# Optimization experiments

Measured on AMD Instinct MI355X. Metric: run time of the kernel, lower is better.

## Reference

```python
import jax, jax.numpy as jnp
import numpy as np

B, H_TRAJ, S = 8, 16, 64
DIM, C = 128, 2000
D = 2 * DIM            # transformer d_model
NUM_HEADS, WINDOW, L = 4, 4, 2
D_FF = 4 * D


def setup_inputs() -> dict:
    key = jax.random.key(0)
    ks = jax.random.split(key, 12)
    w = lambda k, shape, s: jax.random.normal(k, shape, jnp.float32) * s
    return {
        "history": jax.random.randint(ks[0], (B, H_TRAJ, S), 0, C + 1),
        "current_trajectory": jax.random.randint(ks[1], (B, S), 0, C + 1),
        "embedding": w(ks[2], (1, C, DIM), 1.0),
        "null_embedding": jax.random.uniform(ks[3], (D,), jnp.float32),
        "gcn_w": w(ks[4], (DIM, DIM), 0.05),
        "gcn_b": jnp.zeros((DIM,), jnp.float32),
        "enc_attn_w": w(ks[5], (L, 4, D, D), 0.05),
        "enc_attn_b": jnp.zeros((L, 4, D), jnp.float32),
        "enc_ffn_w1": w(ks[6], (L, D, D_FF), 0.05),
        "enc_ffn_b1": jnp.zeros((L, D_FF), jnp.float32),
        "enc_ffn_w2": w(ks[7], (L, D_FF, D), 0.05),
        "enc_ffn_b2": jnp.zeros((L, D), jnp.float32),
        "enc_ln_s": jnp.ones((L, 2, D), jnp.float32),
        "enc_ln_b": jnp.zeros((L, 2, D), jnp.float32),
        "wca_w": w(ks[8], (4, D, D), 0.05),
        "wca_b": jnp.zeros((4, D), jnp.float32),
        "ial_w": w(ks[9], (D, DIM), 0.05),
        "ial_b": jnp.zeros((DIM,), jnp.float32),
    }


def _layer_norm(x, s, b, eps=1e-5):
    m = x.mean(-1, keepdims=True)
    v = ((x - m) ** 2).mean(-1, keepdims=True)
    return (x - m) * jax.lax.rsqrt(v + eps) * s + b


def _mha(xq, xkv, w, b, mask):
    # w: (4,d,d) q/k/v/out, b: (4,d); mask additive, broadcast over heads
    d = xq.shape[-1]
    hd = d // NUM_HEADS
    proj = lambda x, i: (x @ w[i] + b[i]).reshape(x.shape[:-1] + (NUM_HEADS, hd))
    q, k, v = proj(xq, 0), proj(xkv, 1), proj(xkv, 2)
    s = jnp.einsum('bqhd,bkhd->bhqk', q, k) / float(np.sqrt(hd))
    s = s + mask[:, None, :, :]
    a = jax.nn.softmax(s, axis=-1)
    o = jnp.einsum('bhqk,bkhd->bqhd', a, v).reshape(xq.shape)
    return o @ w[3] + b[3]


def _get_graph(history):
    # vectorized scatter-add replacement of the python triple loop
    src, dst = history[:, :, :-1], history[:, :, 1:]
    h_idx = jnp.arange(H_TRAJ, dtype=jnp.float32)
    wts = 1.0 + jnp.exp(-0.01 * (H_TRAJ - 1 - h_idx))          # per-trajectory weight
    valid = (src != C) & (dst != C) & (src != dst)
    wv = jnp.where(valid, wts[None, :, None], 0.0)
    sc, dc = jnp.clip(src, 0, C - 1), jnp.clip(dst, 0, C - 1)
    flat = (jnp.arange(B)[:, None, None] * C * C + sc * C + dc).ravel()
    A = jnp.zeros((B * C * C,), jnp.float32).at[flat].add(wv.ravel())
    return A.reshape(B, C, C)


def _mytransform(A):
    A = A + jnp.eye(C, dtype=A.dtype)
    d = jnp.sqrt(A.sum(axis=1))          # torch code: sqrt of dim-1 sums (no inverse)
    return d[:, :, None] * A * d[:, None, :]   # D @ A @ D


def _temporal(seq_len, d):
    t = jnp.arange(seq_len, dtype=jnp.float32)[:, None]
    den = 10000.0 ** (jnp.arange(0, d, 2, dtype=jnp.float32) / d)
    arg = t / den[None, :]
    return jnp.stack([jnp.sin(arg), jnp.cos(arg)], axis=-1).reshape(seq_len, d)


def _fuse(pos, hist, temp, null_emb):
    # pos: (B,C,D); hist: (B,...,S); gather + where fusion
    g = jax.vmap(lambda p, h: p[h])(pos, jnp.clip(hist, 0, C - 1))
    return jnp.where((hist == C)[..., None], null_emb + temp, g + temp)


def _encoder(x, mask, aw, ab, fw1, fb1, fw2, fb2, lns, lnb):
    for l in range(L):
        a = _mha(x, x, aw[l], ab[l], mask)
        x = _layer_norm(x + a, lns[l, 0], lnb[l, 0])
        f = jax.nn.relu(x @ fw1[l] + fb1[l]) @ fw2[l] + fb2[l]
        x = _layer_norm(x + f, lns[l, 1], lnb[l, 1])
    return x


def reference(history, current_trajectory, embedding, null_embedding, gcn_w, gcn_b,
              enc_attn_w, enc_attn_b, enc_ffn_w1, enc_ffn_b1, enc_ffn_w2, enc_ffn_b2,
              enc_ln_s, enc_ln_b, wca_w, wca_b, ial_w, ial_b):
    E = jnp.broadcast_to(embedding, (B, C, DIM))
    A = _mytransform(_get_graph(history))                      # (B,C,C)
    Eg = jax.nn.relu(A @ E @ gcn_w + gcn_b)                    # GCN layer
    pos = jnp.concatenate([E, Eg], axis=-1)                    # (B,C,2*dim)
    temp = _temporal(S, D)
    fh = _fuse(pos, history, temp, null_embedding).reshape(B * H_TRAJ, S, D)
    fc = _fuse(pos, current_trajectory, temp, null_embedding)  # (B,S,D)
    hmask = jnp.broadcast_to(
        jnp.where((history == C)[:, :, None, :], -jnp.inf, 0.0),
        (B, H_TRAJ, S, S)).reshape(B * H_TRAJ, S, S)
    cmask = jnp.broadcast_to(
        jnp.where((current_trajectory == C)[:, None, :], -jnp.inf, 0.0), (B, S, S))
    mh = _encoder(fh, hmask, enc_attn_w, enc_attn_b, enc_ffn_w1, enc_ffn_b1,
                  enc_ffn_w2, enc_ffn_b2, enc_ln_s, enc_ln_b)
    mc = _encoder(fc, cmask, enc_attn_w, enc_attn_b, enc_ffn_w1, enc_ffn_b1,
                  enc_ffn_w2, enc_ffn_b2, enc_ln_s, enc_ln_b)
    cur_rep = jnp.broadcast_to(mc[:, None], (B, H_TRAJ, S, D)).reshape(B * H_TRAJ, S, D)
    i = jnp.arange(S)
    wmask = jnp.where(jnp.abs(i[:, None] - i[None, :]) <= WINDOW, 0.0, -jnp.inf)[None]
    wca = mh + _mha(mh, cur_rep, wca_w, wca_b, wmask)          # window-based cross attn
    wca = wca.reshape(B, H_TRAJ, S, D)
    # information aggregation over the trajectory axis
    scores = jnp.einsum('bhsd,bsd->bhs', wca, mc) / float(np.sqrt(D))
    aw = jax.nn.softmax(scores, axis=1)
    agg = jnp.einsum('bhs,bhsd->bsd', aw, wca)
    final = jax.nn.relu((agg + mc) @ ial_w + ial_b)            # (B,S,dim)
    return final @ embedding[0].T                              # (B,S,C)
```

## Files before the change

### kernel.cpp

```cpp
#include <hip/hip_runtime.h>
#include <hip/hip_bf16.h>
#include <math.h>

#define C_N   2000
#define DIMN  128
#define DM    256
#define B_N   8
#define HT    16
#define S_N   64
#define NSEQ  136
#define DFF   1024
#define NEDGE (B_N*HT*(S_N-1))

typedef __hip_bfloat16 bf16;
typedef short bf16x8 __attribute__((ext_vector_type(8)));
typedef float f32x4  __attribute__((ext_vector_type(4)));

#define GLOAD_LDS16(gp, lp) \
    __builtin_amdgcn_global_load_lds((const __attribute__((address_space(1))) void*)(gp), \
                                     (__attribute__((address_space(3))) void*)(lp), 16, 0, 0)

__device__ __forceinline__ short f2bf(float v) {
    bf16 t = (bf16)v;
    return *reinterpret_cast<short*>(&t);
}


__global__ void k_colsum(const int* __restrict__ hist, float* __restrict__ colsum) {
    int e = blockIdx.x * blockDim.x + threadIdx.x;
    if (e >= NEDGE) return;
    int s = e % (S_N-1); int bh = e / (S_N-1); int h = bh % HT; int b = bh / HT;
    const int* row = hist + (size_t)bh * S_N;
    int src = row[s], dst = row[s+1];
    if (src != C_N && dst != C_N && src != dst) {
        float w = 1.f + expf(-0.01f * (float)(HT - 1 - h));
        atomicAdd(&colsum[b * C_N + dst], w);
    }
}

__global__ void k_dsqrt(float* __restrict__ dv) {
    int i = blockIdx.x * blockDim.x + threadIdx.x;
    if (i < B_N * C_N) dv[i] = sqrtf(1.f + dv[i]);
}

__global__ void k_initX(const float* __restrict__ dv, const float* __restrict__ E,
                        float* __restrict__ X) {
    size_t i = (size_t)blockIdx.x * 256 + threadIdx.x;
    int k = (int)(i % DIMN); size_t bc = i / DIMN;
    int c = (int)(bc % C_N); int b = (int)(bc / C_N);
    float dd = dv[b * C_N + c];
    X[i] = dd * dd * E[(size_t)c * DIMN + k];
}

__global__ void k_edgeX(const int* __restrict__ hist, const float* __restrict__ dv,
                        const float* __restrict__ E, float* __restrict__ X) {
    int e = blockIdx.x;
    int s = e % (S_N-1); int bh = e / (S_N-1); int h = bh % HT; int b = bh / HT;
    const int* row = hist + (size_t)bh * S_N;
    int src = row[s], dst = row[s+1];
    if (src == C_N || dst == C_N || src == dst) return;
    float w = (1.f + expf(-0.01f * (float)(HT - 1 - h))) * dv[b*C_N+src] * dv[b*C_N+dst];
    int k = threadIdx.x;
    atomicAdd(&X[((size_t)b * C_N + src) * DIMN + k], w * E[(size_t)dst * DIMN + k]);
}


__global__ void k_tobf(const float* __restrict__ s, bf16* __restrict__ d, int n) {
    int i = (blockIdx.x * 256 + threadIdx.x) * 4;
    if (i >= n) return;
    float4 v = *(const float4*)(s + i);
    d[i]   = (bf16)v.x; d[i+1] = (bf16)v.y; d[i+2] = (bf16)v.z; d[i+3] = (bf16)v.w;
}

__global__ void k_transp(const float* __restrict__ src, bf16* __restrict__ dst, int K, int N) {
    __shared__ float t[32][33];
    int mat = blockIdx.z;
    const float* s = src + (size_t)mat * K * N;
    bf16* d = dst + (size_t)mat * N * K;
    int k0 = blockIdx.y * 32, n0 = blockIdx.x * 32;
    #pragma unroll
    for (int j = 0; j < 32; j += 8)
        t[threadIdx.y + j][threadIdx.x] = s[(size_t)(k0 + threadIdx.y + j) * N + n0 + threadIdx.x];
    __syncthreads();
    #pragma unroll
    for (int j = 0; j < 32; j += 8)
        d[(size_t)(n0 + threadIdx.y + j) * K + k0 + threadIdx.x] = (bf16)t[threadIdx.x][threadIdx.y + j];
}

template<int EPI>
__global__ __launch_bounds__(256) void k_bgemm(
        const bf16* __restrict__ A, const bf16* __restrict__ Bt,
        const float* __restrict__ bias, const float* __restrict__ resid,
        void* __restrict__ Cout, int M, int N, int K)
{
    __shared__ bf16 As[128 * 64];
    __shared__ bf16 Bs[64 * 64];
    int tid = threadIdx.x;
    int wid = tid >> 6, lane = tid & 63;
    int m0 = blockIdx.y * 128, n0 = blockIdx.x * 64;
    int wr = wid >> 1, wc = wid & 1;
    int lr = lane >> 3, lc = lane & 7;
    int gc = lc ^ lr;
    f32x4 acc[4][2] = {};

    int nkt = K >> 6;
    for (int kt = 0; kt < nkt; ++kt) {
        int kb = kt << 6;
        #pragma unroll
        for (int s = 0; s < 4; ++s) {
            int seg = wid * 4 + s;
            int row = seg * 8 + lr;
            GLOAD_LDS16(A + (size_t)(m0 + row) * K + kb + gc * 8, As + seg * 512);
        }
        #pragma unroll
        for (int s = 0; s < 2; ++s) {
            int seg = wid * 2 + s;
            int row = seg * 8 + lr;
            GLOAD_LDS16(Bt + (size_t)(n0 + row) * K + kb + gc * 8, Bs + seg * 512);
        }
        __syncthreads();
        #pragma unroll
        for (int kk = 0; kk < 2; ++kk) {
            bf16x8 af[4], bfr[2];
            int c = kk * 4 + (lane >> 4);
            #pragma unroll
            for (int m = 0; m < 4; ++m) {
                int row = wr * 64 + m * 16 + (lane & 15);
                af[m] = *(const bf16x8*)(As + row * 64 + (c ^ (row & 7)) * 8);
            }
            #pragma unroll
            for (int n = 0; n < 2; ++n) {
                int row = wc * 32 + n * 16 + (lane & 15);
                bfr[n] = *(const bf16x8*)(Bs + row * 64 + (c ^ (row & 7)) * 8);
            }
            #pragma unroll
            for (int m = 0; m < 4; ++m)
                #pragma unroll
                for (int n = 0; n < 2; ++n)
                    acc[m][n] = __builtin_amdgcn_mfma_f32_16x16x32_bf16(af[m], bfr[n], acc[m][n], 0, 0, 0);
        }
        __syncthreads();
    }
    int cl = lane & 15, ch = lane >> 4;
    #pragma unroll
    for (int n = 0; n < 2; ++n) {
        int col = n0 + wc * 32 + n * 16 + cl;
        float bv = bias[col];
        #pragma unroll
        for (int m = 0; m < 4; ++m) {
            #pragma unroll
            for (int j = 0; j < 4; ++j) {
                int row = m0 + wr * 64 + m * 16 + ch * 4 + j;
                float v = acc[m][n][j] + bv;
                if (EPI & 4) v += resid[(size_t)row * N + col];
                if (EPI & 2) v = fmaxf(v, 0.f);
                if (EPI & 8) ((bf16*)Cout)[(size_t)row * N + col] = (bf16)v;
                else         ((float*)Cout)[(size_t)row * N + col] = v;
            }
        }
    }
}

template<int EPI, bool BTRANS>
__global__ __launch_bounds__(256) void k_gemm(
        const float* __restrict__ A, const float* __restrict__ Bm,
        const float* __restrict__ bias, const float* __restrict__ resid,
        float* __restrict__ Cm, int M, int N, int K)
{
    __shared__ float As[16][65];
    __shared__ float Bs[16][65];
    int tid = threadIdx.x;
    int tx = tid & 15, ty = tid >> 4;
    int m0 = blockIdx.y * 64, n0 = blockIdx.x * 64;
    float acc[4][4] = {};
    for (int k0 = 0; k0 < K; k0 += 16) {
        {
            int mm = tid >> 2;
            int kk = (tid & 3) << 2;
            int m = m0 + mm;
            float4 v = {0,0,0,0};
            if (m < M) v = *(const float4*)(A + (size_t)m * K + k0 + kk);
            As[kk+0][mm] = v.x; As[kk+1][mm] = v.y; As[kk+2][mm] = v.z; As[kk+3][mm] = v.w;
        }
        if (!BTRANS) {
            int kk = tid >> 4;
            int nn = (tid & 15) << 2;
            int n = n0 + nn;
            const float* src = Bm + (size_t)(k0+kk) * N + n;
            float4 v = {0,0,0,0};
            if (n + 3 < N) v = *(const float4*)src;
            else {
                if (n   < N) v.x = src[0];
                if (n+1 < N) v.y = src[1];
                if (n+2 < N) v.z = src[2];
                if (n+3 < N) v.w = src[3];
            }
            Bs[kk][nn] = v.x; Bs[kk][nn+1] = v.y; Bs[kk][nn+2] = v.z; Bs[kk][nn+3] = v.w;
        } else {
            int nn = tid >> 2;
            int kk = (tid & 3) << 2;
            int n = n0 + nn;
            float4 v = {0,0,0,0};
            if (n < N) v = *(const float4*)(Bm + (size_t)n * K + k0 + kk);
            Bs[kk+0][nn] = v.x; Bs[kk+1][nn] = v.y; Bs[kk+2][nn] = v.z; Bs[kk+3][nn] = v.w;
        }
        __syncthreads();
        #pragma unroll
        for (int kk = 0; kk < 16; ++kk) {
            float a[4], b[4];
            #pragma unroll
            for (int i = 0; i < 4; ++i) a[i] = As[kk][ty*4+i];
            #pragma unroll
            for (int j = 0; j < 4; ++j) b[j] = Bs[kk][tx*4+j];
            #pragma unroll
            for (int i = 0; i < 4; ++i)
                #pragma unroll
                for (int j = 0; j < 4; ++j)
                    acc[i][j] = fmaf(a[i], b[j], acc[i][j]);
        }
        __syncthreads();
    }
    #pragma unroll
    for (int i = 0; i < 4; ++i) {
        int m = m0 + ty*4 + i;
        if (m >= M) continue;
        #pragma unroll
        for (int j = 0; j < 4; ++j) {
            int n = n0 + tx*4 + j;
            if (n >= N) continue;
            float v = acc[i][j];
            if (EPI & 1) v += bias[n];
            if (EPI & 4) v += resid[(size_t)m * N + n];
            if (EPI & 2) v = fmaxf(v, 0.f);
            Cm[(size_t)m * N + n] = v;
        }
    }
}


__global__ void k_temp(float* __restrict__ temp) {
    int s = blockIdx.x; int d = threadIdx.x;
    int k = d >> 1;
    float den = powf(10000.f, (2.f * (float)k) / 256.f);
    float arg = (float)s / den;
    temp[s * DM + d] = (d & 1) ? cosf(arg) : sinf(arg);
}

__global__ void k_fuse(const int* __restrict__ hist, const int* __restrict__ cur,
                       const float* __restrict__ E, const float* __restrict__ Eg,
                       const float* __restrict__ nullE, const float* __restrict__ temp,
                       float* __restrict__ Xenc, bf16* __restrict__ Xbf,
                       float* __restrict__ maskb) {
    int blk = blockIdx.x;
    int seq = blk >> 6, s = blk & 63;
    int d = threadIdx.x;
    int idx, b;
    if (seq < 128) { b = seq >> 4; idx = hist[(size_t)seq * S_N + s]; }
    else           { b = seq - 128; idx = cur[b * S_N + s]; }
    float t = temp[s * DM + d];
    float v;
    if (idx == C_N) v = nullE[d] + t;
    else {
        v = ((d < DIMN) ? E[(size_t)idx * DIMN + d]
                        : Eg[((size_t)b * C_N + idx) * DIMN + (d - DIMN)]) + t;
    }
    size_t o = ((size_t)seq * S_N + s) * DM + d;
    Xenc[o] = v;
    Xbf[o]  = (bf16)v;
    if (d == 0) maskb[seq * S_N + s] = (idx == C_N) ? -INFINITY : 0.f;
}

template<bool WCA>
__global__ __launch_bounds__(64) void k_mattn(
        const bf16* __restrict__ Qb, const bf16* __restrict__ Kb,
        const bf16* __restrict__ Vb, const float* __restrict__ maskb,
        bf16* __restrict__ O, int qstr, int kstr)
{
    int seq = blockIdx.x >> 2, head = blockIdx.x & 3;
    int lane = threadIdx.x;
    int cl = lane & 15, ch = lane >> 4;
    __shared__ __align__(16) short VT[64 * 72];
    __shared__ __align__(16) short PT[64 * 72];

    const bf16* Qp = Qb + (size_t)seq * 64 * qstr + head * 64;
    int kvseq = WCA ? (seq >> 4) : seq;
    const bf16* Kp = Kb + (size_t)kvseq * 64 * kstr + head * 64;
    const bf16* Vp = Vb + (size_t)kvseq * 64 * kstr + head * 64;

    bf16x8 aq[4][2], bk[4][2], vr[4][2];
    #pragma unroll
    for (int t = 0; t < 4; ++t)
        #pragma unroll
        for (int kk = 0; kk < 2; ++kk) {
            int row = t * 16 + cl, d0 = kk * 32 + ch * 8;
            aq[t][kk] = *(const bf16x8*)(Qp + (size_t)row * qstr + d0);
            bk[t][kk] = *(const bf16x8*)(Kp + (size_t)row * kstr + d0);
            vr[t][kk] = *(const bf16x8*)(Vp + (size_t)row * kstr + d0);
        }

    f32x4 sa[4][4] = {};
    #pragma unroll
    for (int kk = 0; kk < 2; ++kk)
        #pragma unroll
        for (int m = 0; m < 4; ++m)
            #pragma unroll
            for (int n = 0; n < 4; ++n)
                sa[m][n] = __builtin_amdgcn_mfma_f32_16x16x32_bf16(aq[m][kk], bk[n][kk], sa[m][n], 0, 0, 0);

    #pragma unroll
    for (int t = 0; t < 4; ++t)
        #pragma unroll
        for (int kk = 0; kk < 2; ++kk) {
            int k = t * 16 + cl, d0 = kk * 32 + ch * 8;
            #pragma unroll
            for (int e = 0; e < 8; ++e)
                VT[(d0 + e) * 72 + k] = vr[t][kk][e];
        }

    float mk4[4];
    if (!WCA) {
        #pragma unroll
        for (int n = 0; n < 4; ++n) mk4[n] = maskb[seq * 64 + n * 16 + cl];
    }

    #pragma unroll
    for (int m = 0; m < 4; ++m) {
        #pragma unroll
        for (int j = 0; j < 4; ++j) {
            int q = m * 16 + ch * 4 + j;
            float rm = -INFINITY;
            #pragma unroll
            for (int n = 0; n < 4; ++n) {
                int k = n * 16 + cl;
                float msk = WCA ? ((abs(q - k) <= 4) ? 0.f : -INFINITY) : mk4[n];
                float v = sa[m][n][j] * 0.125f + msk;
                sa[m][n][j] = v;
                rm = fmaxf(rm, v);
            }
            rm = fmaxf(rm, __shfl_xor(rm, 1));
            rm = fmaxf(rm, __shfl_xor(rm, 2));
            rm = fmaxf(rm, __shfl_xor(rm, 4));
            rm = fmaxf(rm, __shfl_xor(rm, 8));
            float rs = 0.f;
            #pragma unroll
            for (int n = 0; n < 4; ++n) {
                float e = expf(sa[m][n][j] - rm);
                sa[m][n][j] = e;
                rs += e;
            }
            rs += __shfl_xor(rs, 1);
            rs += __shfl_xor(rs, 2);
            rs += __shfl_xor(rs, 4);
            rs += __shfl_xor(rs, 8);
            float inv = 1.f / rs;
            #pragma unroll
            for (int n = 0; n < 4; ++n)
                PT[q * 72 + n * 16 + cl] = f2bf(sa[m][n][j] * inv);
        }
    }
    __syncthreads();

    f32x4 oa[4][4] = {};
    #pragma unroll
    for (int kk = 0; kk < 2; ++kk) {
        bf16x8 av[4], bp[4];
        #pragma unroll
        for (int dm = 0; dm < 4; ++dm)
            av[dm] = *(const bf16x8*)(VT + (dm * 16 + cl) * 72 + kk * 32 + ch * 8);
        #pragma unroll
        for (int qn = 0; qn < 4; ++qn)
            bp[qn] = *(const bf16x8*)(PT + (qn * 16 + cl) * 72 + kk * 32 + ch * 8);
        #pragma unroll
        for (int dm = 0; dm < 4; ++dm)
            #pragma unroll
            for (int qn = 0; qn < 4; ++qn)
                oa[dm][qn] = __builtin_amdgcn_mfma_f32_16x16x32_bf16(av[dm], bp[qn], oa[dm][qn], 0, 0, 0);
    }
    __syncthreads();

    #pragma unroll
    for (int dm = 0; dm < 4; ++dm)
        #pragma unroll
        for (int qn = 0; qn < 4; ++qn)
            #pragma unroll
            for (int j = 0; j < 4; ++j)
                PT[(qn * 16 + cl) * 72 + dm * 16 + ch * 4 + j] = f2bf(oa[dm][qn][j]);
    __syncthreads();
    #pragma unroll
    for (int it = 0; it < 8; ++it) {
        int chunk = it * 64 + lane;
        int tok = chunk >> 3, d0 = (chunk & 7) * 8;
        bf16x8 v = *(const bf16x8*)(PT + tok * 72 + d0);
        *(bf16x8*)(O + ((size_t)seq * 64 + tok) * 256 + head * 64 + d0) = v;
    }
}


__global__ __launch_bounds__(256) void k_ln(float* __restrict__ x, const float* __restrict__ a,
                                            const float* __restrict__ s, const float* __restrict__ b,
                                            bf16* __restrict__ xbf) {
    int row = blockIdx.x;
    int d = threadIdx.x;
    size_t idx = (size_t)row * DM + d;
    float v = x[idx] + a[idx];
    __shared__ float red[8];
    float t = v;
    #pragma unroll
    for (int o = 1; o < 64; o <<= 1) t += __shfl_xor(t, o);
    if ((d & 63) == 0) red[d >> 6] = t;
    __syncthreads();
    float mean = (red[0] + red[1] + red[2] + red[3]) * (1.f / 256.f);
    float c = v - mean;
    float t2 = c * c;
    #pragma unroll
    for (int o = 1; o < 64; o <<= 1) t2 += __shfl_xor(t2, o);
    if ((d & 63) == 0) red[4 + (d >> 6)] = t2;
    __syncthreads();
    float var = (red[4] + red[5] + red[6] + red[7]) * (1.f / 256.f);
    float r = c * rsqrtf(var + 1e-5f) * s[d] + b[d];
    x[idx] = r;
    xbf[idx] = (bf16)r;
}


__global__ __launch_bounds__(256) void k_agg(const float* __restrict__ wca,
                                             const float* __restrict__ mc,
                                             float* __restrict__ aggmc) {
    int bs = blockIdx.x; int b = bs >> 6, s = bs & 63;
    int d = threadIdx.x;
    __shared__ float sc[16];
    __shared__ float red[4];
    float mcv = mc[((size_t)b * S_N + s) * DM + d];
    float wv[16];
    #pragma unroll
    for (int h = 0; h < 16; ++h) {
        float w = wca[(((size_t)(b * HT + h)) * S_N + s) * DM + d];
        wv[h] = w;
        float t = w * mcv;
        #pragma unroll
        for (int o = 1; o < 64; o <<= 1) t += __shfl_xor(t, o);
        if ((d & 63) == 0) red[d >> 6] = t;
        __syncthreads();
        if (d == 0) sc[h] = (red[0] + red[1] + red[2] + red[3]) * (1.f / 16.f);
        __syncthreads();
    }
    float mx = -INFINITY;
    #pragma unroll
    for (int h = 0; h < 16; ++h) mx = fmaxf(mx, sc[h]);
    float e[16]; float sum = 0.f;
    #pragma unroll
    for (int h = 0; h < 16; ++h) { e[h] = expf(sc[h] - mx); sum += e[h]; }
    float inv = 1.f / sum;
    float acc = 0.f;
    #pragma unroll
    for (int h = 0; h < 16; ++h) acc += e[h] * inv * wv[h];
    aggmc[((size_t)b * S_N + s) * DM + d] = acc + mcv;
}


extern "C" void kernel_launch(void* const* d_in, const int* in_sizes, int n_in,
                              void* d_out, int out_size, void* d_ws, size_t ws_size,
                              hipStream_t stream) {
    const int*   history = (const int*)d_in[0];
    const int*   cur     = (const int*)d_in[1];
    const float* emb     = (const float*)d_in[2];
    const float* nullE   = (const float*)d_in[3];
    const float* gcn_w   = (const float*)d_in[4];
    const float* gcn_b   = (const float*)d_in[5];
    const float* aw      = (const float*)d_in[6];
    const float* ab      = (const float*)d_in[7];
    const float* fw1     = (const float*)d_in[8];
    const float* fb1     = (const float*)d_in[9];
    const float* fw2     = (const float*)d_in[10];
    const float* fb2     = (const float*)d_in[11];
    const float* lns     = (const float*)d_in[12];
    const float* lnb     = (const float*)d_in[13];
    const float* wca_w   = (const float*)d_in[14];
    const float* wca_b   = (const float*)d_in[15];
    const float* ial_w   = (const float*)d_in[16];
    const float* ial_b   = (const float*)d_in[17];
    float* out = (float*)d_out;
    float* ws  = (float*)d_ws;

    float* dvec   = ws + 0;
    float* maskb  = ws + 16000;
    float* temp   = ws + 24704;
    float* aggmc  = ws + 41088;
    float* finalb = ws + 172160;
    bf16*  wbf    = (bf16*)(ws + 237696);
    float* Xenc   = ws + 1163392;
    bf16*  Xbf    = (bf16*)(ws + 3391616);
    bf16*  Abf    = (bf16*)(ws + 4505728);
    bf16*  Hbf    = (bf16*)(ws + 5619840);
    bf16*  QKVbf  = (bf16*)(ws + 10076288);
    float* O2     = ws + 13418624;
    float* SE     = ws + 15646848;

    bf16* wbf_aw  = wbf;
    bf16* wbf_fw1 = wbf + 524288;
    bf16* wbf_fw2 = wbf + 1048576;
    bf16* wbf_wca = wbf + 1572864;
    bf16* wbf_gcn = wbf + 1835008;

    float* Xg   = O2;
    bf16*  Xgbf = Hbf;
    float* Eg   = SE;
    bf16*  Qwbf = QKVbf;
    bf16*  KVbf = QKVbf + 4194304;

    k_transp<<<dim3(8, 8, 8),  dim3(32, 8), 0, stream>>>(aw,    wbf_aw, 256, 256);
    k_transp<<<dim3(32, 8, 2), dim3(32, 8), 0, stream>>>(fw1,   wbf_fw1, 256, 1024);
    k_transp<<<dim3(8, 32, 2), dim3(32, 8), 0, stream>>>(fw2,   wbf_fw2, 1024, 256);
    k_transp<<<dim3(8, 8, 4),  dim3(32, 8), 0, stream>>>(wca_w, wbf_wca, 256, 256);
    k_transp<<<dim3(4, 4, 1),  dim3(32, 8), 0, stream>>>(gcn_w, wbf_gcn, 128, 128);

    hipMemsetAsync(dvec, 0, 16000 * sizeof(float), stream);
    k_colsum<<<(NEDGE + 255) / 256, 256, 0, stream>>>(history, dvec);
    k_dsqrt<<<(B_N * C_N + 255) / 256, 256, 0, stream>>>(dvec);
    k_initX<<<B_N * C_N * DIMN / 256, 256, 0, stream>>>(dvec, emb, Xg);
    k_edgeX<<<NEDGE, 128, 0, stream>>>(history, dvec, emb, Xg);
    k_tobf<<<2000, 256, 0, stream>>>(Xg, Xgbf, B_N * C_N * DIMN);
    k_bgemm<2><<<dim3(2, 125), 256, 0, stream>>>(Xgbf, wbf_gcn, gcn_b, nullptr, Eg,
                                                 B_N * C_N, DIMN, DIMN);

    k_temp<<<S_N, DM, 0, stream>>>(temp);
    k_fuse<<<NSEQ * S_N, DM, 0, stream>>>(history, cur, emb, Eg, nullE, temp, Xenc, Xbf, maskb);

    for (int l = 0; l < 2; ++l) {
        k_bgemm<9><<<dim3(12, 68), 256, 0, stream>>>(Xbf, wbf_aw + l * 262144,
                ab + l * 1024, nullptr, QKVbf, NSEQ * S_N, 768, 256);
        k_mattn<false><<<NSEQ * 4, 64, 0, stream>>>(QKVbf, QKVbf + 256, QKVbf + 512,
                maskb, Abf, 768, 768);
        k_bgemm<0><<<dim3(4, 68), 256, 0, stream>>>(Abf, wbf_aw + l * 262144 + 196608,
                ab + l * 1024 + 768, nullptr, O2, NSEQ * S_N, 256, 256);
        k_ln<<<NSEQ * S_N, DM, 0, stream>>>(Xenc, O2, lns + (l * 2 + 0) * DM, lnb + (l * 2 + 0) * DM, Xbf);
        k_bgemm<10><<<dim3(16, 68), 256, 0, stream>>>(Xbf, wbf_fw1 + l * 262144,
                fb1 + l * DFF, nullptr, Hbf, NSEQ * S_N, DFF, 256);
        k_bgemm<0><<<dim3(4, 68), 256, 0, stream>>>(Hbf, wbf_fw2 + l * 262144,
                fb2 + l * DM, nullptr, O2, NSEQ * S_N, 256, 1024);
        k_ln<<<NSEQ * S_N, DM, 0, stream>>>(Xenc, O2, lns + (l * 2 + 1) * DM, lnb + (l * 2 + 1) * DM, Xbf);
    }

    float* mh = Xenc;
    bf16*  mc_bf = Xbf + (size_t)128 * S_N * DM;

    k_bgemm<9><<<dim3(4, 64), 256, 0, stream>>>(Xbf, wbf_wca, wca_b, nullptr, Qwbf,
                                                128 * S_N, 256, 256);
    k_bgemm<9><<<dim3(8, 4), 256, 0, stream>>>(mc_bf, wbf_wca + 65536, wca_b + 256, nullptr, KVbf,
                                               B_N * S_N, 512, 256);
    k_mattn<true><<<128 * 4, 64, 0, stream>>>(Qwbf, KVbf, KVbf + 256, nullptr, Abf, 256, 512);
    k_bgemm<4><<<dim3(4, 64), 256, 0, stream>>>(Abf, wbf_wca + 196608, wca_b + 768, mh, SE,
                                                128 * S_N, 256, 256);

    k_agg<<<B_N * S_N, DM, 0, stream>>>(SE, Xenc + (size_t)128 * S_N * DM, aggmc);
    k_gemm<3, false><<<dim3(2, 8), 256, 0, stream>>>(aggmc, ial_w, ial_b, nullptr, finalb,
                                                     B_N * S_N, DIMN, DM);
    k_gemm<0, true><<<dim3(32, 8), 256, 0, stream>>>(finalb, emb, nullptr, nullptr, out,
                                                     B_N * S_N, C_N, DIMN);
}
```

Measured before the change: 380.6 us.

## Reassociate GCN, fuse GEMM with LayerNorm, move tail GEMMs to MFMA

The GCN is reassociated so the embedding is multiplied by the GCN weight once (2000 rows instead of 16000), and the degree scaling and edge scatter are applied to that product, with bias added and ReLU deferred to the fuse kernel. Output-projection and FFN2 GEMMs are fused with the residual add and LayerNorm in a new full-row kernel, which removes the separate LN passes and the O2 round trip. Weight transposes are packed into one launch, the aggregation kernel reduces all 16 scores in one pass instead of syncing per trajectory, and the final two fp32 SIMT GEMMs become bf16 MFMA GEMMs with a padded embedding. The fused LN uses a single-pass variance, and the extra bf16 rounding in the tail may change numerics slightly.

```diff
diff --git a/kernel.cpp b/kernel.cpp
--- a/kernel.cpp
+++ b/kernel.cpp
@@ -38,30 +38,26 @@
     }
 }
 
-__global__ void k_dsqrt(float* __restrict__ dv) {
-    int i = blockIdx.x * blockDim.x + threadIdx.x;
-    if (i < B_N * C_N) dv[i] = sqrtf(1.f + dv[i]);
-}
-
-__global__ void k_initX(const float* __restrict__ dv, const float* __restrict__ E,
-                        float* __restrict__ X) {
+__global__ void k_initX(const float* __restrict__ cs, const float* __restrict__ Y,
+                        const float* __restrict__ gb, float* __restrict__ Eg) {
     size_t i = (size_t)blockIdx.x * 256 + threadIdx.x;
     int k = (int)(i % DIMN); size_t bc = i / DIMN;
     int c = (int)(bc % C_N); int b = (int)(bc / C_N);
-    float dd = dv[b * C_N + c];
-    X[i] = dd * dd * E[(size_t)c * DIMN + k];
-}
-
-__global__ void k_edgeX(const int* __restrict__ hist, const float* __restrict__ dv,
-                        const float* __restrict__ E, float* __restrict__ X) {
+    float dd2 = 1.f + cs[b * C_N + c];
+    Eg[i] = dd2 * Y[(size_t)c * DIMN + k] + gb[k];
+}
+
+__global__ void k_edgeX(const int* __restrict__ hist, const float* __restrict__ cs,
+                        const float* __restrict__ Y, float* __restrict__ Eg) {
     int e = blockIdx.x;
     int s = e % (S_N-1); int bh = e / (S_N-1); int h = bh % HT; int b = bh / HT;
     const int* row = hist + (size_t)bh * S_N;
     int src = row[s], dst = row[s+1];
     if (src == C_N || dst == C_N || src == dst) return;
-    float w = (1.f + expf(-0.01f * (float)(HT - 1 - h))) * dv[b*C_N+src] * dv[b*C_N+dst];
+    float w = (1.f + expf(-0.01f * (float)(HT - 1 - h)))
+            * sqrtf(1.f + cs[b*C_N+src]) * sqrtf(1.f + cs[b*C_N+dst]);
     int k = threadIdx.x;
-    atomicAdd(&X[((size_t)b * C_N + src) * DIMN + k], w * E[(size_t)dst * DIMN + k]);
+    atomicAdd(&Eg[((size_t)b * C_N + src) * DIMN + k], w * Y[(size_t)dst * DIMN + k]);
 }
 
 
@@ -72,26 +68,39 @@
     d[i]   = (bf16)v.x; d[i+1] = (bf16)v.y; d[i+2] = (bf16)v.z; d[i+3] = (bf16)v.w;
 }
 
-__global__ void k_transp(const float* __restrict__ src, bf16* __restrict__ dst, int K, int N) {
+struct TEnt { const float* s; bf16* d; int K; int N; int nm; int tiles; };
+struct TPack { TEnt e[6]; };
+
+__global__ void k_wtpack(TPack p) {
     __shared__ float t[32][33];
-    int mat = blockIdx.z;
-    const float* s = src + (size_t)mat * K * N;
-    bf16* d = dst + (size_t)mat * N * K;
-    int k0 = blockIdx.y * 32, n0 = blockIdx.x * 32;
+    int id = blockIdx.x;
+    TEnt en = p.e[0];
+    #pragma unroll
+    for (int k = 0; k < 6; ++k) {
+        if (id < p.e[k].tiles) { en = p.e[k]; break; }
+        id -= p.e[k].tiles;
+    }
+    int tn = en.N >> 5;
+    int per = (en.K >> 5) * tn;
+    int mat = id / per, t2 = id % per;
+    int ty = t2 / tn, tx = t2 % tn;
+    const float* s = en.s + (size_t)mat * en.K * en.N;
+    bf16* d = en.d + (size_t)mat * en.N * en.K;
+    int k0 = ty * 32, n0 = tx * 32;
     #pragma unroll
     for (int j = 0; j < 32; j += 8)
-        t[threadIdx.y + j][threadIdx.x] = s[(size_t)(k0 + threadIdx.y + j) * N + n0 + threadIdx.x];
+        t[threadIdx.y + j][threadIdx.x] = s[(size_t)(k0 + threadIdx.y + j) * en.N + n0 + threadIdx.x];
     __syncthreads();
     #pragma unroll
     for (int j = 0; j < 32; j += 8)
-        d[(size_t)(n0 + threadIdx.y + j) * K + k0 + threadIdx.x] = (bf16)t[threadIdx.x][threadIdx.y + j];
+        d[(size_t)(n0 + threadIdx.y + j) * en.K + k0 + threadIdx.x] = (bf16)t[threadIdx.x][threadIdx.y + j];
 }
 
 template<int EPI>
 __global__ __launch_bounds__(256) void k_bgemm(
         const bf16* __restrict__ A, const bf16* __restrict__ Bt,
         const float* __restrict__ bias, const float* __restrict__ resid,
-        void* __restrict__ Cout, int M, int N, int K)
+        void* __restrict__ Cout, int M, int N, int K, int ldc, int nreal)
 {
     __shared__ bf16 As[128 * 64];
     __shared__ bf16 Bs[64 * 64];
@@ -145,94 +154,113 @@
     #pragma unroll
     for (int n = 0; n < 2; ++n) {
         int col = n0 + wc * 32 + n * 16 + cl;
-        float bv = bias[col];
+        if ((EPI & 16) && col >= nreal) continue;
+        float bv = (EPI & 1) ? bias[col] : 0.f;
         #pragma unroll
         for (int m = 0; m < 4; ++m) {
             #pragma unroll
             for (int j = 0; j < 4; ++j) {
                 int row = m0 + wr * 64 + m * 16 + ch * 4 + j;
                 float v = acc[m][n][j] + bv;
-                if (EPI & 4) v += resid[(size_t)row * N + col];
+                if (EPI & 4) v += resid[(size_t)row * ldc + col];
                 if (EPI & 2) v = fmaxf(v, 0.f);
-                if (EPI & 8) ((bf16*)Cout)[(size_t)row * N + col] = (bf16)v;
-                else         ((float*)Cout)[(size_t)row * N + col] = v;
-            }
-        }
-    }
-}
-
-template<int EPI, bool BTRANS>
-__global__ __launch_bounds__(256) void k_gemm(
-        const float* __restrict__ A, const float* __restrict__ Bm,
-        const float* __restrict__ bias, const float* __restrict__ resid,
-        float* __restrict__ Cm, int M, int N, int K)
+                if (EPI & 8) ((bf16*)Cout)[(size_t)row * ldc + col] = (bf16)v;
+                else         ((float*)Cout)[(size_t)row * ldc + col] = v;
+            }
+        }
+    }
+}
+
+__global__ __launch_bounds__(256) void k_bgemm_ln(
+        const bf16* __restrict__ A, const bf16* __restrict__ Bt,
+        const float* __restrict__ bias, float* __restrict__ Xf,
+        const float* __restrict__ lns_, const float* __restrict__ lnb_,
+        bf16* __restrict__ Xb, int M, int K)
 {
-    __shared__ float As[16][65];
-    __shared__ float Bs[16][65];
-    int tid = threadIdx.x;
-    int tx = tid & 15, ty = tid >> 4;
-    int m0 = blockIdx.y * 64, n0 = blockIdx.x * 64;
-    float acc[4][4] = {};
-    for (int k0 = 0; k0 < K; k0 += 16) {
-        {
-            int mm = tid >> 2;
-            int kk = (tid & 3) << 2;
-            int m = m0 + mm;
-            float4 v = {0,0,0,0};
-            if (m < M) v = *(const float4*)(A + (size_t)m * K + k0 + kk);
-            As[kk+0][mm] = v.x; As[kk+1][mm] = v.y; As[kk+2][mm] = v.z; As[kk+3][mm] = v.w;
-        }
-        if (!BTRANS) {
-            int kk = tid >> 4;
-            int nn = (tid & 15) << 2;
-            int n = n0 + nn;
-            const float* src = Bm + (size_t)(k0+kk) * N + n;
-            float4 v = {0,0,0,0};
-            if (n + 3 < N) v = *(const float4*)src;
-            else {
-                if (n   < N) v.x = src[0];
-                if (n+1 < N) v.y = src[1];
-                if (n+2 < N) v.z = src[2];
-                if (n+3 < N) v.w = src[3];
-            }
-            Bs[kk][nn] = v.x; Bs[kk][nn+1] = v.y; Bs[kk][nn+2] = v.z; Bs[kk][nn+3] = v.w;
-        } else {
-            int nn = tid >> 2;
-            int kk = (tid & 3) << 2;
-            int n = n0 + nn;
-            float4 v = {0,0,0,0};
-            if (n < N) v = *(const float4*)(Bm + (size_t)n * K + k0 + kk);
-            Bs[kk+0][nn] = v.x; Bs[kk+1][nn] = v.y; Bs[kk+2][nn] = v.z; Bs[kk+3][nn] = v.w;
+    __shared__ bf16 As[64 * 64];
+    __shared__ bf16 Bs[256 * 64];
+    __shared__ float ls1[64][4], ls2[64][4];
+    int tid = threadIdx.x, wid = tid >> 6, lane = tid & 63;
+    int lr = lane >> 3, lc = lane & 7, gc = lc ^ lr;
+    int cl = lane & 15, ch = lane >> 4;
+    int m0 = blockIdx.x * 64;
+    int wc = wid;
+    f32x4 acc[4][4] = {};
+    int nkt = K >> 6;
+    for (int kt = 0; kt < nkt; ++kt) {
+        int kb = kt << 6;
+        #pragma unroll
+        for (int s = 0; s < 2; ++s) {
+            int seg = wid * 2 + s, row = seg * 8 + lr;
+            GLOAD_LDS16(A + (size_t)(m0 + row) * K + kb + gc * 8, As + seg * 512);
+        }
+        #pragma unroll
+        for (int s = 0; s < 8; ++s) {
+            int seg = wid * 8 + s, row = seg * 8 + lr;
+            GLOAD_LDS16(Bt + (size_t)row * K + kb + gc * 8, Bs + seg * 512);
         }
         __syncthreads();
         #pragma unroll
-        for (int kk = 0; kk < 16; ++kk) {
-            float a[4], b[4];
-            #pragma unroll
-            for (int i = 0; i < 4; ++i) a[i] = As[kk][ty*4+i];
-            #pragma unroll
-            for (int j = 0; j < 4; ++j) b[j] = Bs[kk][tx*4+j];
-            #pragma unroll
-            for (int i = 0; i < 4; ++i)
+        for (int kk = 0; kk < 2; ++kk) {
+            int c = kk * 4 + ch;
+            bf16x8 af[4], bfr[4];
+            #pragma unroll
+            for (int m = 0; m < 4; ++m) {
+                int row = m * 16 + cl;
+                af[m] = *(const bf16x8*)(As + row * 64 + (c ^ (row & 7)) * 8);
+            }
+            #pragma unroll
+            for (int n = 0; n < 4; ++n) {
+                int row = wc * 64 + n * 16 + cl;
+                bfr[n] = *(const bf16x8*)(Bs + row * 64 + (c ^ (row & 7)) * 8);
+            }
+            #pragma unroll
+            for (int m = 0; m < 4; ++m)
                 #pragma unroll
-                for (int j = 0; j < 4; ++j)
-                    acc[i][j] = fmaf(a[i], b[j], acc[i][j]);
+                for (int n = 0; n < 4; ++n)
+                    acc[m][n] = __builtin_amdgcn_mfma_f32_16x16x32_bf16(af[m], bfr[n], acc[m][n], 0, 0, 0);
         }
         __syncthreads();
     }
     #pragma unroll
-    for (int i = 0; i < 4; ++i) {
-        int m = m0 + ty*4 + i;
-        if (m >= M) continue;
+    for (int m = 0; m < 4; ++m) {
         #pragma unroll
         for (int j = 0; j < 4; ++j) {
-            int n = n0 + tx*4 + j;
-            if (n >= N) continue;
-            float v = acc[i][j];
-            if (EPI & 1) v += bias[n];
-            if (EPI & 4) v += resid[(size_t)m * N + n];
-            if (EPI & 2) v = fmaxf(v, 0.f);
-            Cm[(size_t)m * N + n] = v;
+            int rl = m * 16 + ch * 4 + j;
+            float s1 = 0.f, s2 = 0.f;
+            #pragma unroll
+            for (int n = 0; n < 4; ++n) {
+                int col = wc * 64 + n * 16 + cl;
+                float v = acc[m][n][j] + bias[col] + Xf[(size_t)(m0 + rl) * 256 + col];
+                acc[m][n][j] = v;
+                s1 += v; s2 += v * v;
+            }
+            s1 += __shfl_xor(s1, 1); s2 += __shfl_xor(s2, 1);
+            s1 += __shfl_xor(s1, 2); s2 += __shfl_xor(s2, 2);
+            s1 += __shfl_xor(s1, 4); s2 += __shfl_xor(s2, 4);
+            s1 += __shfl_xor(s1, 8); s2 += __shfl_xor(s2, 8);
+            if (cl == 0) { ls1[rl][wc] = s1; ls2[rl][wc] = s2; }
+        }
+    }
+    __syncthreads();
+    #pragma unroll
+    for (int m = 0; m < 4; ++m) {
+        #pragma unroll
+        for (int j = 0; j < 4; ++j) {
+            int rl = m * 16 + ch * 4 + j;
+            float su = ls1[rl][0] + ls1[rl][1] + ls1[rl][2] + ls1[rl][3];
+            float sq = ls2[rl][0] + ls2[rl][1] + ls2[rl][2] + ls2[rl][3];
+            float mean = su * (1.f / 256.f);
+            float var  = sq * (1.f / 256.f) - mean * mean;
+            float rstd = rsqrtf(var + 1e-5f);
+            #pragma unroll
+            for (int n = 0; n < 4; ++n) {
+                int col = wc * 64 + n * 16 + cl;
+                float r = (acc[m][n][j] - mean) * rstd * lns_[col] + lnb_[col];
+                size_t g = (size_t)(m0 + rl) * 256 + col;
+                Xf[g] = r;
+                Xb[g] = (bf16)r;
+            }
         }
     }
 }
@@ -262,7 +290,7 @@
     if (idx == C_N) v = nullE[d] + t;
     else {
         v = ((d < DIMN) ? E[(size_t)idx * DIMN + d]
-                        : Eg[((size_t)b * C_N + idx) * DIMN + (d - DIMN)]) + t;
+                        : fmaxf(Eg[((size_t)b * C_N + idx) * DIMN + (d - DIMN)], 0.f)) + t;
     }
     size_t o = ((size_t)seq * S_N + s) * DM + d;
     Xenc[o] = v;
@@ -396,65 +424,43 @@
 }
 
 
-__global__ __launch_bounds__(256) void k_ln(float* __restrict__ x, const float* __restrict__ a,
-                                            const float* __restrict__ s, const float* __restrict__ b,
-                                            bf16* __restrict__ xbf) {
-    int row = blockIdx.x;
-    int d = threadIdx.x;
-    size_t idx = (size_t)row * DM + d;
-    float v = x[idx] + a[idx];
-    __shared__ float red[8];
-    float t = v;
-    #pragma unroll
-    for (int o = 1; o < 64; o <<= 1) t += __shfl_xor(t, o);
-    if ((d & 63) == 0) red[d >> 6] = t;
-    __syncthreads();
-    float mean = (red[0] + red[1] + red[2] + red[3]) * (1.f / 256.f);
-    float c = v - mean;
-    float t2 = c * c;
-    #pragma unroll
-    for (int o = 1; o < 64; o <<= 1) t2 += __shfl_xor(t2, o);
-    if ((d & 63) == 0) red[4 + (d >> 6)] = t2;
-    __syncthreads();
-    float var = (red[4] + red[5] + red[6] + red[7]) * (1.f / 256.f);
-    float r = c * rsqrtf(var + 1e-5f) * s[d] + b[d];
-    x[idx] = r;
-    xbf[idx] = (bf16)r;
-}
-
-
 __global__ __launch_bounds__(256) void k_agg(const float* __restrict__ wca,
                                              const float* __restrict__ mc,
-                                             float* __restrict__ aggmc) {
+                                             bf16* __restrict__ aggbf) {
     int bs = blockIdx.x; int b = bs >> 6, s = bs & 63;
     int d = threadIdx.x;
-    __shared__ float sc[16];
-    __shared__ float red[4];
+    __shared__ float red[4][16];
     float mcv = mc[((size_t)b * S_N + s) * DM + d];
-    float wv[16];
+    float wv[16], p[16];
     #pragma unroll
     for (int h = 0; h < 16; ++h) {
-        float w = wca[(((size_t)(b * HT + h)) * S_N + s) * DM + d];
-        wv[h] = w;
-        float t = w * mcv;
-        #pragma unroll
-        for (int o = 1; o < 64; o <<= 1) t += __shfl_xor(t, o);
-        if ((d & 63) == 0) red[d >> 6] = t;
-        __syncthreads();
-        if (d == 0) sc[h] = (red[0] + red[1] + red[2] + red[3]) * (1.f / 16.f);
-        __syncthreads();
-    }
-    float mx = -INFINITY;
-    #pragma unroll
-    for (int h = 0; h < 16; ++h) mx = fmaxf(mx, sc[h]);
-    float e[16]; float sum = 0.f;
+        wv[h] = wca[(((size_t)(b * HT + h)) * S_N + s) * DM + d];
+        p[h] = wv[h] * mcv;
+    }
+    #pragma unroll
+    for (int o = 1; o < 64; o <<= 1)
+        #pragma unroll
+        for (int h = 0; h < 16; ++h) p[h] += __shfl_xor(p[h], o);
+    if ((d & 63) == 0) {
+        int w = d >> 6;
+        #pragma unroll
+        for (int h = 0; h < 16; ++h) red[w][h] = p[h];
+    }
+    __syncthreads();
+    float sc[16], mx = -INFINITY;
+    #pragma unroll
+    for (int h = 0; h < 16; ++h) {
+        sc[h] = (red[0][h] + red[1][h] + red[2][h] + red[3][h]) * (1.f / 16.f);
+        mx = fmaxf(mx, sc[h]);
+    }
+    float e[16], sum = 0.f;
     #pragma unroll
     for (int h = 0; h < 16; ++h) { e[h] = expf(sc[h] - mx); sum += e[h]; }
     float inv = 1.f / sum;
     float acc = 0.f;
     #pragma unroll
     for (int h = 0; h < 16; ++h) acc += e[h] * inv * wv[h];
-    aggmc[((size_t)b * S_N + s) * DM + d] = acc + mcv;
+    aggbf[((size_t)b * S_N + s) * DM + d] = (bf16)(acc + mcv);
 }
 
 
@@ -485,76 +491,80 @@
     float* dvec   = ws + 0;
     float* maskb  = ws + 16000;
     float* temp   = ws + 24704;
-    float* aggmc  = ws + 41088;
-    float* finalb = ws + 172160;
-    bf16*  wbf    = (bf16*)(ws + 237696);
-    float* Xenc   = ws + 1163392;
-    bf16*  Xbf    = (bf16*)(ws + 3391616);
-    bf16*  Abf    = (bf16*)(ws + 4505728);
-    bf16*  Hbf    = (bf16*)(ws + 5619840);
-    bf16*  QKVbf  = (bf16*)(ws + 10076288);
-    float* O2     = ws + 13418624;
-    float* SE     = ws + 15646848;
+    bf16*  aggbf  = (bf16*)(ws + 41088);
+    bf16*  finalb = (bf16*)(ws + 106624);
+    bf16*  embbf  = (bf16*)(ws + 139392);
+    float* Y      = ws + 270464;
+    float* Eg     = ws + 532608;
+    bf16*  wbf    = (bf16*)(ws + 2580608);
+    float* Xenc   = ws + 3522688;
+    bf16*  Xbf    = (bf16*)(ws + 5750912);
+    bf16*  Abf    = (bf16*)(ws + 6865024);
+    bf16*  Hbf    = (bf16*)(ws + 7979136);
+    bf16*  QKVbf  = (bf16*)(ws + 12435584);
+    float* SE     = ws + 15777920;
 
     bf16* wbf_aw  = wbf;
     bf16* wbf_fw1 = wbf + 524288;
     bf16* wbf_fw2 = wbf + 1048576;
     bf16* wbf_wca = wbf + 1572864;
     bf16* wbf_gcn = wbf + 1835008;
-
-    float* Xg   = O2;
-    bf16*  Xgbf = Hbf;
-    float* Eg   = SE;
-    bf16*  Qwbf = QKVbf;
-    bf16*  KVbf = QKVbf + 4194304;
-
-    k_transp<<<dim3(8, 8, 8),  dim3(32, 8), 0, stream>>>(aw,    wbf_aw, 256, 256);
-    k_transp<<<dim3(32, 8, 2), dim3(32, 8), 0, stream>>>(fw1,   wbf_fw1, 256, 1024);
-    k_transp<<<dim3(8, 32, 2), dim3(32, 8), 0, stream>>>(fw2,   wbf_fw2, 1024, 256);
-    k_transp<<<dim3(8, 8, 4),  dim3(32, 8), 0, stream>>>(wca_w, wbf_wca, 256, 256);
-    k_transp<<<dim3(4, 4, 1),  dim3(32, 8), 0, stream>>>(gcn_w, wbf_gcn, 128, 128);
+    bf16* wbf_ial = wbf + 1851392;
+
+    bf16* Qwbf = QKVbf;
+    bf16* KVbf = QKVbf + 4194304;
+
+    TPack tp;
+    tp.e[0] = { aw,    wbf_aw,  256,  256, 8, 512 };
+    tp.e[1] = { fw1,   wbf_fw1, 256, 1024, 2, 512 };
+    tp.e[2] = { fw2,   wbf_fw2, 1024, 256, 2, 512 };
+    tp.e[3] = { wca_w, wbf_wca, 256,  256, 4, 256 };
+    tp.e[4] = { gcn_w, wbf_gcn, 128,  128, 1,  16 };
+    tp.e[5] = { ial_w, wbf_ial, 256,  128, 1,  32 };
+    k_wtpack<<<1840, dim3(32, 8), 0, stream>>>(tp);
+
+    hipMemsetAsync(embbf + 2000 * 128, 0, 48 * 128 * sizeof(bf16), stream);
+    k_tobf<<<250, 256, 0, stream>>>(emb, embbf, C_N * DIMN);
 
     hipMemsetAsync(dvec, 0, 16000 * sizeof(float), stream);
     k_colsum<<<(NEDGE + 255) / 256, 256, 0, stream>>>(history, dvec);
-    k_dsqrt<<<(B_N * C_N + 255) / 256, 256, 0, stream>>>(dvec);
-    k_initX<<<B_N * C_N * DIMN / 256, 256, 0, stream>>>(dvec, emb, Xg);
-    k_edgeX<<<NEDGE, 128, 0, stream>>>(history, dvec, emb, Xg);
-    k_tobf<<<2000, 256, 0, stream>>>(Xg, Xgbf, B_N * C_N * DIMN);
-    k_bgemm<2><<<dim3(2, 125), 256, 0, stream>>>(Xgbf, wbf_gcn, gcn_b, nullptr, Eg,
-                                                 B_N * C_N, DIMN, DIMN);
+    k_bgemm<0><<<dim3(2, 16), 256, 0, stream>>>(embbf, wbf_gcn, nullptr, nullptr, Y,
+                                                2048, DIMN, DIMN, DIMN, DIMN);
+    k_initX<<<B_N * C_N * DIMN / 256, 256, 0, stream>>>(dvec, Y, gcn_b, Eg);
+    k_edgeX<<<NEDGE, 128, 0, stream>>>(history, dvec, Y, Eg);
 
     k_temp<<<S_N, DM, 0, stream>>>(temp);
     k_fuse<<<NSEQ * S_N, DM, 0, stream>>>(history, cur, emb, Eg, nullE, temp, Xenc, Xbf, maskb);
 
     for (int l = 0; l < 2; ++l) {
         k_bgemm<9><<<dim3(12, 68), 256, 0, stream>>>(Xbf, wbf_aw + l * 262144,
-                ab + l * 1024, nullptr, QKVbf, NSEQ * S_N, 768, 256);
+                ab + l * 1024, nullptr, QKVbf, NSEQ * S_N, 768, 256, 768, 768);
         k_mattn<false><<<NSEQ * 4, 64, 0, stream>>>(QKVbf, QKVbf + 256, QKVbf + 512,
                 maskb, Abf, 768, 768);
-        k_bgemm<0><<<dim3(4, 68), 256, 0, stream>>>(Abf, wbf_aw + l * 262144 + 196608,
-                ab + l * 1024 + 768, nullptr, O2, NSEQ * S_N, 256, 256);
-        k_ln<<<NSEQ * S_N, DM, 0, stream>>>(Xenc, O2, lns + (l * 2 + 0) * DM, lnb + (l * 2 + 0) * DM, Xbf);
-        k_bgemm<10><<<dim3(16, 68), 256, 0, stream>>>(Xbf, wbf_fw1 + l * 262144,
-                fb1 + l * DFF, nullptr, Hbf, NSEQ * S_N, DFF, 256);
-        k_bgemm<0><<<dim3(4, 68), 256, 0, stream>>>(Hbf, wbf_fw2 + l * 262144,
-                fb2 + l * DM, nullptr, O2, NSEQ * S_N, 256, 1024);
-        k_ln<<<NSEQ * S_N, DM, 0, stream>>>(Xenc, O2, lns + (l * 2 + 1) * DM, lnb + (l * 2 + 1) * DM, Xbf);
+        k_bgemm_ln<<<NSEQ, 256, 0, stream>>>(Abf, wbf_aw + l * 262144 + 196608,
+                ab + l * 1024 + 768, Xenc, lns + (l * 2 + 0) * DM, lnb + (l * 2 + 0) * DM,
+                Xbf, NSEQ * S_N, 256);
+        k_bgemm<11><<<dim3(16, 68), 256, 0, stream>>>(Xbf, wbf_fw1 + l * 262144,
+                fb1 + l * DFF, nullptr, Hbf, NSEQ * S_N, DFF, 256, DFF, DFF);
+        k_bgemm_ln<<<NSEQ, 256, 0, stream>>>(Hbf, wbf_fw2 + l * 262144,
+                fb2 + l * DM, Xenc, lns + (l * 2 + 1) * DM, lnb + (l * 2 + 1) * DM,
+                Xbf, NSEQ * S_N, 1024);
     }
 
     float* mh = Xenc;
     bf16*  mc_bf = Xbf + (size_t)128 * S_N * DM;
 
     k_bgemm<9><<<dim3(4, 64), 256, 0, stream>>>(Xbf, wbf_wca, wca_b, nullptr, Qwbf,
-                                                128 * S_N, 256, 256);
-    k_bgemm<9><<<dim3(8, 4), 256, 0, stream>>>(mc_bf, wbf_wca + 65536, wca_b + 256, nullptr, KVbf,
-                                               B_N * S_N, 512, 256);
+                                                128 * S_N, 256, 256, 256, 256);
+    k_bgemm<9><<<dim3(8, 4), 256, 0, stream>>>(mc_bf, wbf_wca + 65536, wca_b + 256, nullptr,
+                                               KVbf, B_N * S_N, 512, 256, 512, 512);
     k_mattn<true><<<128 * 4, 64, 0, stream>>>(Qwbf, KVbf, KVbf + 256, nullptr, Abf, 256, 512);
-    k_bgemm<4><<<dim3(4, 64), 256, 0, stream>>>(Abf, wbf_wca + 196608, wca_b + 768, mh, SE,
-                                                128 * S_N, 256, 256);
-
-    k_agg<<<B_N * S_N, DM, 0, stream>>>(SE, Xenc + (size_t)128 * S_N * DM, aggmc);
-    k_gemm<3, false><<<dim3(2, 8), 256, 0, stream>>>(aggmc, ial_w, ial_b, nullptr, finalb,
-                                                     B_N * S_N, DIMN, DM);
-    k_gemm<0, true><<<dim3(32, 8), 256, 0, stream>>>(finalb, emb, nullptr, nullptr, out,
-                                                     B_N * S_N, C_N, DIMN);
-}
+    k_bgemm<5><<<dim3(4, 64), 256, 0, stream>>>(Abf, wbf_wca + 196608, wca_b + 768, mh, SE,
+                                                128 * S_N, 256, 256, 256, 256);
+
+    k_agg<<<B_N * S_N, 256, 0, stream>>>(SE, Xenc + (size_t)128 * S_N * DM, aggbf);
+    k_bgemm<11><<<dim3(2, 4), 256, 0, stream>>>(aggbf, wbf_ial, ial_b, nullptr, finalb,
+                                                B_N * S_N, DIMN, DM, DIMN, DIMN);
+    k_bgemm<16><<<dim3(32, 4), 256, 0, stream>>>(finalb, embbf, nullptr, nullptr, out,
+                                                 B_N * S_N, 2048, DIMN, C_N, C_N);
+}
```

Measured after the change: 347.5 us. 1.1x faster.
